# Performance work log

Hardware: AMD Instinct MI355X
Metric: run time of the kernel (lower is better)

The kernel has to match this reference:

```python
import jax, jax.numpy as jnp
import numpy as np

KSZ = 5   # local window size per spatial dim
NH = 4    # num_channels -> attention heads
EPS = 1e-6

def rmsnorm(x, w):
    return x * jax.lax.rsqrt(jnp.mean(x * x, axis=-1, keepdims=True) + EPS) * w

def local_windows(x, ksz):
    # x: [B, D, H, W, C] -> [B, D, H, W, ksz**3, C] zero-padded SAME windows
    B, D, H, Wd, C = x.shape
    xt = jnp.transpose(x, (0, 4, 1, 2, 3))  # NCDHW
    p = jax.lax.conv_general_dilated_patches(xt, (ksz, ksz, ksz), (1, 1, 1), 'SAME')
    p = p.reshape(B, C, ksz ** 3, D, H, Wd)  # channel-major patch layout
    return jnp.transpose(p, (0, 3, 4, 5, 2, 1))

def forward(x, norm1_w, attn_norm_w, norm2_w, wq, wk, wv, wo, gate_w, up_w, down_w):
    B, D, H, Wd, C = x.shape
    hd = C // NH
    k3 = KSZ ** 3
    h = rmsnorm(x, norm1_w)
    q = (h @ wq).reshape(B, D, H, Wd, NH, hd)
    k = h @ wk
    v = h @ wv
    kwin = local_windows(k, KSZ).reshape(B, D, H, Wd, k3, NH, hd)
    vwin = local_windows(v, KSZ).reshape(B, D, H, Wd, k3, NH, hd)
    scores = jnp.einsum('bxyzhe,bxyzkhe->bxyzhk', q, kwin) / jnp.sqrt(jnp.float32(hd))
    ones = jnp.ones((1, D, H, Wd, 1), x.dtype)
    valid = local_windows(ones, KSZ)[..., 0] > 0.5  # [1,D,H,W,k3] padding mask
    scores = jnp.where(valid[:, :, :, :, None, :], scores, jnp.float32(-1e9))
    attn = jax.nn.softmax(scores, axis=-1)
    o = jnp.einsum('bxyzhk,bxyzkhe->bxyzhe', attn, vwin).reshape(B, D, H, Wd, C)
    x = x + rmsnorm(o @ wo, attn_norm_w)
    h2 = rmsnorm(x, norm2_w)
    x = x + (jax.nn.silu(h2 @ gate_w) * (h2 @ up_w)) @ down_w  # SwiGLU (dropout=eval)
    return x

def setup_inputs():
    key = jax.random.key(0)
    ks = jax.random.split(key, 8)
    width, hidden = 128, 512
    s = 0.02
    return {
        'x': jax.random.normal(ks[0], (1, 16, 16, 16, width), jnp.float32),
        'norm1_w': jnp.ones((width,), jnp.float32),
        'attn_norm_w': jnp.ones((width,), jnp.float32),
        'norm2_w': jnp.ones((width,), jnp.float32),
        'wq': jax.random.normal(ks[1], (width, width), jnp.float32) * s,
        'wk': jax.random.normal(ks[2], (width, width), jnp.float32) * s,
        'wv': jax.random.normal(ks[3], (width, width), jnp.float32) * s,
        'wo': jax.random.normal(ks[4], (width, width), jnp.float32) * s,
        'gate_w': jax.random.normal(ks[5], (width, hidden), jnp.float32) * s,
        'up_w': jax.random.normal(ks[6], (width, hidden), jnp.float32) * s,
        'down_w': jax.random.normal(ks[7], (hidden, width), jnp.float32) * s,
    }

def reference(x, norm1_w, attn_norm_w, norm2_w, wq, wk, wv, wo, gate_w, up_w, down_w):
    return forward(x, norm1_w, attn_norm_w, norm2_w, wq, wk, wv, wo, gate_w, up_w, down_w)
```

## Files before the change

### kernel.cpp

```cpp
#include <hip/hip_runtime.h>
#include <hip/hip_bf16.h>

#define NVOX 4096
#define C    128
#define HID  512
#define EPSF 1e-6f

typedef __attribute__((ext_vector_type(8))) short bf16x8;
typedef __attribute__((ext_vector_type(4))) float f32x4;

__device__ __forceinline__ short f2bs(float f) {
    __hip_bfloat16 h = __float2bfloat16(f);
    short s; __builtin_memcpy(&s, &h, 2); return s;
}
__device__ __forceinline__ float bs2f(unsigned short u) {
    return __uint_as_float(((unsigned)u) << 16);
}

__device__ __forceinline__ bf16x8 lda(const short* hs, int lane, int ks) {
    int r = lane & 15, g = lane >> 4;
    int col = (ks * 32 + g * 8) ^ ((r & 7) << 3);
    return *(const bf16x8*)(hs + r * 128 + col);
}

__device__ __forceinline__ float wave_rsum(float s) {
    s += __shfl_xor(s, 32); s += __shfl_xor(s, 16); s += __shfl_xor(s, 8);
    s += __shfl_xor(s, 4);  s += __shfl_xor(s, 2);  s += __shfl_xor(s, 1);
    return s;
}

__global__ __launch_bounds__(512) void k_prep(
    const float* __restrict__ wq, const float* __restrict__ wk,
    const float* __restrict__ wv, const float* __restrict__ wo,
    const float* __restrict__ gw, const float* __restrict__ uw,
    const float* __restrict__ dw, short* __restrict__ wsw)
{
    int id = blockIdx.x * 512 + threadIdx.x;
    const float* src; int base, ct, ks, lane, N, KS;
    if (id < 8192) {
        int m = id >> 11, loc = id & 2047;
        src = (m == 0) ? wq : (m == 1) ? wk : (m == 2) ? wv : wo;
        base = m << 14; N = 128; KS = 4;
        ct = loc >> 8; ks = (loc >> 6) & 3; lane = loc & 63;
    } else if (id < 16384) {
        int loc = id - 8192;
        src = gw; base = 65536; N = 512; KS = 4;
        ct = loc >> 8; ks = (loc >> 6) & 3; lane = loc & 63;
    } else if (id < 24576) {
        int loc = id - 16384;
        src = uw; base = 131072; N = 512; KS = 4;
        ct = loc >> 8; ks = (loc >> 6) & 3; lane = loc & 63;
    } else {
        int loc = id - 24576;
        src = dw; base = 196608; N = 128; KS = 16;
        ct = loc >> 10; ks = (loc >> 6) & 15; lane = loc & 63;
    }
    int k0 = ks * 32 + (lane >> 4) * 8;
    int c  = ct * 16 + (lane & 15);
    bf16x8 v;
    #pragma unroll
    for (int j = 0; j < 8; j++) v[j] = f2bs(src[(size_t)(k0 + j) * N + c]);
    *(bf16x8*)(wsw + base + (((ct * KS + ks) * 64 + lane) << 3)) = v;
}

__global__ __launch_bounds__(256) void k_qkv(
    const float* __restrict__ x, const float* __restrict__ n1,
    const short* __restrict__ wsw,
    short* __restrict__ qbf, short* __restrict__ kbf, short* __restrict__ vbf)
{
    __shared__ short hs[2048];
    const int r0 = blockIdx.x * 16, t = threadIdx.x;
    const int w = t >> 6, lane = t & 63;

    #pragma unroll
    for (int i = 0; i < 4; i++) {
        int r = w * 4 + i;
        const float* xp = x + (size_t)(r0 + r) * 128;
        float v0 = xp[lane], v1 = xp[lane + 64];
        float s = wave_rsum(fmaf(v0, v0, v1 * v1));
        float sc = rsqrtf(s * (1.0f / 128.0f) + EPSF);
        int p3 = (r & 7) << 3;
        hs[r * 128 + (lane ^ p3)]        = f2bs(v0 * sc * n1[lane]);
        hs[r * 128 + ((lane + 64) ^ p3)] = f2bs(v1 * sc * n1[lane + 64]);
    }
    __syncthreads();

    bf16x8 af[4];
    #pragma unroll
    for (int ks = 0; ks < 4; ks++) af[ks] = lda(hs, lane, ks);

    const int rb = (lane >> 4) * 4, cl = lane & 15;
    #pragma unroll
    for (int m = 0; m < 3; m++) {
        const short* wb = wsw + (m << 14);
        f32x4 a0 = {0.f,0.f,0.f,0.f}, a1 = {0.f,0.f,0.f,0.f};
        #pragma unroll
        for (int ks = 0; ks < 4; ks++) {
            bf16x8 b0 = *(const bf16x8*)(wb + ((((w * 2) * 4 + ks) * 64 + lane) << 3));
            bf16x8 b1 = *(const bf16x8*)(wb + ((((w * 2 + 1) * 4 + ks) * 64 + lane) << 3));
            a0 = __builtin_amdgcn_mfma_f32_16x16x32_bf16(af[ks], b0, a0, 0, 0, 0);
            a1 = __builtin_amdgcn_mfma_f32_16x16x32_bf16(af[ks], b1, a1, 0, 0, 0);
        }
        short* outp = (m == 0) ? qbf : (m == 1) ? kbf : vbf;
        short* hp = outp + (size_t)w * NVOX * 32;
        #pragma unroll
        for (int i = 0; i < 4; i++) {
            hp[(size_t)(r0 + rb + i) * 32 + cl]      = f2bs(a0[i]);
            hp[(size_t)(r0 + rb + i) * 32 + 16 + cl] = f2bs(a1[i]);
        }
    }
}

__global__ __launch_bounds__(256) void k_attn(
    const short* __restrict__ qbf, const short* __restrict__ kbf,
    const short* __restrict__ vbf, short* __restrict__ obf)
{
    __shared__ __align__(16) char smem[64128];
    short* K_lds = (short*)smem;
    short* PA    = (short*)smem;
    short* S_lds = (short*)(smem + 30720);
    short* VB    = (short*)(smem + 30720);
    short* Q_lds = (short*)(smem + 61440);
    float* inv   = (float*)(smem + 64000);

    const int b = blockIdx.x, head = blockIdx.y, t = threadIdx.x;
    const int ow = (b & 3) * 4, oh = ((b >> 2) & 3) * 4, od = (b >> 4) * 2;
    const int w = t >> 6, lane = t & 63;
    const int g = lane >> 4, r = lane & 15;
    const short* kh = kbf + (size_t)head * NVOX * 32;
    const short* vh = vbf + (size_t)head * NVOX * 32;
    const short* qh = qbf + (size_t)head * NVOX * 32;

    uint4 v0[4] = {}, v1[4] = {};
    {
        int row = t;
        int lw = row & 7, lh = (row >> 3) & 7, ld = row >> 6;
        int gd = od - 2 + ld, gh = oh - 2 + lh, gw_ = ow - 2 + lw;
        int sv = (((unsigned)gd < 16u) && ((unsigned)gh < 16u) && ((unsigned)gw_ < 16u));
        size_t off = (size_t)((((gd << 4) | gh) << 4) | gw_) * 32;
        uint4 kc[4];
        #pragma unroll
        for (int c2 = 0; c2 < 4; c2++) {
            kc[c2] = sv ? *(const uint4*)(kh + off + c2 * 8) : (uint4){0,0,0,0};
            v0[c2] = sv ? *(const uint4*)(vh + off + c2 * 8) : (uint4){0,0,0,0};
        }
        #pragma unroll
        for (int c2 = 0; c2 < 4; c2++) *(uint4*)&K_lds[row * 40 + c2 * 8] = kc[c2];

        if (t >= 128) {
            int row1 = t + 128;
            int lw1 = row1 & 7, lh1 = (row1 >> 3) & 7, ld1 = row1 >> 6;
            int gd1 = od - 2 + ld1, gh1 = oh - 2 + lh1, gw1 = ow - 2 + lw1;
            int sv1 = (((unsigned)gd1 < 16u) && ((unsigned)gh1 < 16u) && ((unsigned)gw1 < 16u));
            size_t off1 = (size_t)((((gd1 << 4) | gh1) << 4) | gw1) * 32;
            uint4 kd[4];
            #pragma unroll
            for (int c2 = 0; c2 < 4; c2++) {
                kd[c2] = sv1 ? *(const uint4*)(kh + off1 + c2 * 8) : (uint4){0,0,0,0};
                v1[c2] = sv1 ? *(const uint4*)(vh + off1 + c2 * 8) : (uint4){0,0,0,0};
            }
            #pragma unroll
            for (int c2 = 0; c2 < 4; c2++) *(uint4*)&K_lds[row1 * 40 + c2 * 8] = kd[c2];
        } else {
            int q = t >> 2, c2q = t & 3;
            int gq = ((od + (q >> 4)) << 8) | ((oh + ((q >> 2) & 3)) << 4) | (ow + (q & 3));
            *(uint4*)&Q_lds[q * 40 + c2q * 8] = *(const uint4*)(qh + (size_t)gq * 32 + c2q * 8);
        }
    }
    __syncthreads();

    {
        bf16x8 bq0 = *(const bf16x8*)(Q_lds + r * 40 + g * 8);
        bf16x8 bq1 = *(const bf16x8*)(Q_lds + (16 + r) * 40 + g * 8);
        #pragma unroll
        for (int jj = 0; jj < 6; jj++) {
            int mt = w + jj * 4;
            bf16x8 ak = *(const bf16x8*)(K_lds + (mt * 16 + r) * 40 + g * 8);
            f32x4 a0 = {0.f,0.f,0.f,0.f}, a1 = {0.f,0.f,0.f,0.f};
            a0 = __builtin_amdgcn_mfma_f32_16x16x32_bf16(ak, bq0, a0, 0, 0, 0);
            a1 = __builtin_amdgcn_mfma_f32_16x16x32_bf16(ak, bq1, a1, 0, 0, 0);
            #pragma unroll
            for (int i = 0; i < 4; i++) {
                int key = mt * 16 + g * 4 + i;
                S_lds[key * 40 + r]      = f2bs(a0[i]);
                S_lds[key * 40 + 16 + r] = f2bs(a1[i]);
            }
        }
    }
    __syncthreads();

    {
        const int q = t >> 3, kl = t & 7;
        const int qw_ = q & 3, qh_ = (q >> 2) & 3, qd_ = q >> 4;
        const float isq = 0.17677669529663687f;
        float mx = -1e30f;
        #pragma unroll
        for (int j = 0; j < 48; j++) {
            int k = kl + (j << 3);
            int lw = k & 7, lh = (k >> 3) & 7, ld = k >> 6;
            int ok = ((unsigned)(ld - qd_) <= 4u) & ((unsigned)(lh - qh_) <= 4u)
                   & ((unsigned)(lw - qw_) <= 4u)
                   & ((unsigned)(od - 2 + ld) < 16u) & ((unsigned)(oh - 2 + lh) < 16u)
                   & ((unsigned)(ow - 2 + lw) < 16u);
            float s = bs2f((unsigned short)S_lds[k * 40 + q]) * isq;
            mx = ok ? fmaxf(mx, s) : mx;
        }
        mx = fmaxf(mx, __shfl_xor(mx, 1));
        mx = fmaxf(mx, __shfl_xor(mx, 2));
        mx = fmaxf(mx, __shfl_xor(mx, 4));
        float ssum = 0.f;
        const int pabase = (q >> 4) * 12 * 512 + (q & 15) * 8 + kl;
        #pragma unroll
        for (int j = 0; j < 48; j++) {
            int k = kl + (j << 3);
            int lw = k & 7, lh = (k >> 3) & 7, ld = k >> 6;
            int ok = ((unsigned)(ld - qd_) <= 4u) & ((unsigned)(lh - qh_) <= 4u)
                   & ((unsigned)(lw - qw_) <= 4u)
                   & ((unsigned)(od - 2 + ld) < 16u) & ((unsigned)(oh - 2 + lh) < 16u)
                   & ((unsigned)(ow - 2 + lw) < 16u);
            float s = bs2f((unsigned short)S_lds[k * 40 + q]) * isq;
            float p = ok ? __expf(s - mx) : 0.f;
            ssum += p;
            PA[pabase + (j >> 2) * 512 + (j & 3) * 128] = f2bs(p);
        }
        ssum += __shfl_xor(ssum, 1);
        ssum += __shfl_xor(ssum, 2);
        ssum += __shfl_xor(ssum, 4);
        if (kl == 0) inv[q] = 1.0f / ssum;
    }
    __syncthreads();

    {
        int row = t;
        int ks = row >> 5, g3 = (row >> 3) & 3, j3 = row & 7;
        const unsigned short* u = (const unsigned short*)v0;
        #pragma unroll
        for (int c = 0; c < 32; c++)
            VB[((c >> 4) * 12 + ks) * 512 + g3 * 128 + (c & 15) * 8 + j3] = (short)u[c];
        if (t >= 128) {
            int row1 = t + 128;
            int ks1 = row1 >> 5, g31 = (row1 >> 3) & 3, j31 = row1 & 7;
            const unsigned short* u1 = (const unsigned short*)v1;
            #pragma unroll
            for (int c = 0; c < 32; c++)
                VB[((c >> 4) * 12 + ks1) * 512 + g31 * 128 + (c & 15) * 8 + j31] = (short)u1[c];
        }
    }
    __syncthreads();

    {
        const int mt2 = w >> 1, ct = w & 1;
        f32x4 acc = {0.f,0.f,0.f,0.f};
        #pragma unroll
        for (int ks = 0; ks < 12; ks++) {
            bf16x8 pa = *(const bf16x8*)(PA + (((mt2 * 12 + ks) * 64 + lane) << 3));
            bf16x8 vb = *(const bf16x8*)(VB + (((ct * 12 + ks) * 64 + lane) << 3));
            acc = __builtin_amdgcn_mfma_f32_16x16x32_bf16(pa, vb, acc, 0, 0, 0);
        }
        #pragma unroll
        for (int i = 0; i < 4; i++) {
            int q = mt2 * 16 + g * 4 + i;
            int c = ct * 16 + r;
            int gvox = ((od + (q >> 4)) << 8) | ((oh + ((q >> 2) & 3)) << 4) | (ow + (q & 3));
            obf[(size_t)gvox * 128 + head * 32 + c] = f2bs(acc[i] * inv[q]);
        }
    }
}

__global__ __launch_bounds__(256) void k_post(
    const short* __restrict__ obf, const short* __restrict__ wsw,
    const float* __restrict__ anw, const float* __restrict__ x,
    const float* __restrict__ n2w, float* __restrict__ out)
{
    __shared__ float ybuf[16][132];
    __shared__ float xres[16][128];
    __shared__ short hs[2048];
    __shared__ short gu[16 * 512];

    const int r0 = blockIdx.x * 16, t = threadIdx.x;
    const int w = t >> 6, lane = t & 63;
    const int ar = lane & 15, ag_ = lane >> 4;

    {
        const short* wb = wsw + (3 << 14);
        f32x4 a0 = {0.f,0.f,0.f,0.f}, a1 = {0.f,0.f,0.f,0.f};
        #pragma unroll
        for (int ks = 0; ks < 4; ks++) {
            bf16x8 a = *(const bf16x8*)(obf + (size_t)(r0 + ar) * 128 + ks * 32 + ag_ * 8);
            bf16x8 b0 = *(const bf16x8*)(wb + ((((w * 2) * 4 + ks) * 64 + lane) << 3));
            bf16x8 b1 = *(const bf16x8*)(wb + ((((w * 2 + 1) * 4 + ks) * 64 + lane) << 3));
            a0 = __builtin_amdgcn_mfma_f32_16x16x32_bf16(a, b0, a0, 0, 0, 0);
            a1 = __builtin_amdgcn_mfma_f32_16x16x32_bf16(a, b1, a1, 0, 0, 0);
        }
        #pragma unroll
        for (int i = 0; i < 4; i++) {
            ybuf[ag_ * 4 + i][w * 32 + ar]      = a0[i];
            ybuf[ag_ * 4 + i][w * 32 + 16 + ar] = a1[i];
        }
    }
    __syncthreads();

    #pragma unroll
    for (int i = 0; i < 4; i++) {
        int r = w * 4 + i;
        float y0 = ybuf[r][lane], y1 = ybuf[r][lane + 64];
        float s = wave_rsum(fmaf(y0, y0, y1 * y1));
        float sc = rsqrtf(s * (1.0f / 128.0f) + EPSF);
        const float* xp = x + (size_t)(r0 + r) * 128;
        float xr0 = xp[lane]      + y0 * sc * anw[lane];
        float xr1 = xp[lane + 64] + y1 * sc * anw[lane + 64];
        xres[r][lane] = xr0; xres[r][lane + 64] = xr1;
        float s2 = wave_rsum(fmaf(xr0, xr0, xr1 * xr1));
        float sc2 = rsqrtf(s2 * (1.0f / 128.0f) + EPSF);
        int p3 = (r & 7) << 3;
        hs[r * 128 + (lane ^ p3)]        = f2bs(xr0 * sc2 * n2w[lane]);
        hs[r * 128 + ((lane + 64) ^ p3)] = f2bs(xr1 * sc2 * n2w[lane + 64]);
    }
    __syncthreads();

    {
        const short* gwb = wsw + 65536;
        const short* uwb = wsw + 131072;
        bf16x8 af[4];
        #pragma unroll
        for (int ks = 0; ks < 4; ks++) af[ks] = lda(hs, lane, ks);
        f32x4 ag[8], au[8];
        #pragma unroll
        for (int i = 0; i < 8; i++) { ag[i] = (f32x4){0.f,0.f,0.f,0.f}; au[i] = (f32x4){0.f,0.f,0.f,0.f}; }
        #pragma unroll
        for (int ks = 0; ks < 4; ks++) {
            #pragma unroll
            for (int i = 0; i < 8; i++) {
                int ct = w * 8 + i;
                bf16x8 bg = *(const bf16x8*)(gwb + (((ct * 4 + ks) * 64 + lane) << 3));
                bf16x8 bu = *(const bf16x8*)(uwb + (((ct * 4 + ks) * 64 + lane) << 3));
                ag[i] = __builtin_amdgcn_mfma_f32_16x16x32_bf16(af[ks], bg, ag[i], 0, 0, 0);
                au[i] = __builtin_amdgcn_mfma_f32_16x16x32_bf16(af[ks], bu, au[i], 0, 0, 0);
            }
        }
        #pragma unroll
        for (int i = 0; i < 8; i++) {
            int col = (w * 8 + i) * 16 + ar;
            #pragma unroll
            for (int j = 0; j < 4; j++) {
                int row = ag_ * 4 + j;
                float g = ag[i][j], uu = au[i][j];
                float sg = g / (1.0f + __expf(-g));
                gu[row * 512 + (col ^ ((row & 7) << 3))] = f2bs(sg * uu);
            }
        }
    }
    __syncthreads();

    {
        const short* db = wsw + 196608;
        f32x4 a0 = {0.f,0.f,0.f,0.f}, a1 = {0.f,0.f,0.f,0.f};
        #pragma unroll
        for (int ks = 0; ks < 16; ks++) {
            int col = (ks * 32 + ag_ * 8) ^ ((ar & 7) << 3);
            bf16x8 a = *(const bf16x8*)(gu + ar * 512 + col);
            bf16x8 b0 = *(const bf16x8*)(db + ((((w * 2) * 16 + ks) * 64 + lane) << 3));
            bf16x8 b1 = *(const bf16x8*)(db + ((((w * 2 + 1) * 16 + ks) * 64 + lane) << 3));
            a0 = __builtin_amdgcn_mfma_f32_16x16x32_bf16(a, b0, a0, 0, 0, 0);
            a1 = __builtin_amdgcn_mfma_f32_16x16x32_bf16(a, b1, a1, 0, 0, 0);
        }
        #pragma unroll
        for (int i = 0; i < 4; i++) {
            int row = ag_ * 4 + i;
            size_t i0 = (size_t)(r0 + row) * 128 + w * 32 + ar;
            out[i0]      = xres[row][w * 32 + ar]      + a0[i];
            out[i0 + 16] = xres[row][w * 32 + 16 + ar] + a1[i];
        }
    }
}

extern "C" void kernel_launch(void* const* d_in, const int* in_sizes, int n_in,
                              void* d_out, int out_size, void* d_ws, size_t ws_size,
                              hipStream_t stream)
{
    const float* x   = (const float*)d_in[0];
    const float* n1  = (const float*)d_in[1];
    const float* anw = (const float*)d_in[2];
    const float* n2  = (const float*)d_in[3];
    const float* wq  = (const float*)d_in[4];
    const float* wk  = (const float*)d_in[5];
    const float* wv  = (const float*)d_in[6];
    const float* wo  = (const float*)d_in[7];
    const float* gw  = (const float*)d_in[8];
    const float* uw  = (const float*)d_in[9];
    const float* dw  = (const float*)d_in[10];
    float* out = (float*)d_out;

    float* ws = (float*)d_ws;
    short* qbf = (short*)ws;
    short* kbf = (short*)(ws + 262144);
    short* vbf = (short*)(ws + 524288);
    short* obf = (short*)(ws + 786432);
    short* wsw = (short*)(ws + 1048576);

    k_prep<<<64,  512, 0, stream>>>(wq, wk, wv, wo, gw, uw, dw, wsw);
    k_qkv <<<256, 256, 0, stream>>>(x, n1, wsw, qbf, kbf, vbf);
    dim3 ga(128, 4);
    k_attn<<<ga,  256, 0, stream>>>(qbf, kbf, vbf, obf);
    k_post<<<256, 256, 0, stream>>>(obf, wsw, anw, x, n2, out);
}
```

Before: 37.50 us.

## Overlap weight conversion with QKV, transpose score layout, head-major attention output

Shrinks the weight-prep kernel to only the Q/K/V weights and moves conversion of wo, gate, up and down weights into the QKV kernel, spread across its blocks, so that work overlaps the QKV projection and the prep kernel finishes sooner. The attention score buffer is transposed to query-major, so each thread writes packed 64-bit stores and reads its scores with vector loads. The validity mask is computed once and kept in a bitmask rather than recomputed in the second softmax pass. The attention output is stored head-major, and the post kernel's A-operand loads change to match. The risk is extra register pressure and tail work in the QKV kernel.

```diff
diff --git a/kernel.cpp b/kernel.cpp
--- a/kernel.cpp
+++ b/kernel.cpp
@@ -31,46 +31,50 @@
 
 __global__ __launch_bounds__(512) void k_prep(
     const float* __restrict__ wq, const float* __restrict__ wk,
-    const float* __restrict__ wv, const float* __restrict__ wo,
-    const float* __restrict__ gw, const float* __restrict__ uw,
-    const float* __restrict__ dw, short* __restrict__ wsw)
+    const float* __restrict__ wv, short* __restrict__ wsw)
 {
     int id = blockIdx.x * 512 + threadIdx.x;
-    const float* src; int base, ct, ks, lane, N, KS;
-    if (id < 8192) {
-        int m = id >> 11, loc = id & 2047;
-        src = (m == 0) ? wq : (m == 1) ? wk : (m == 2) ? wv : wo;
-        base = m << 14; N = 128; KS = 4;
-        ct = loc >> 8; ks = (loc >> 6) & 3; lane = loc & 63;
-    } else if (id < 16384) {
-        int loc = id - 8192;
-        src = gw; base = 65536; N = 512; KS = 4;
-        ct = loc >> 8; ks = (loc >> 6) & 3; lane = loc & 63;
-    } else if (id < 24576) {
-        int loc = id - 16384;
-        src = uw; base = 131072; N = 512; KS = 4;
-        ct = loc >> 8; ks = (loc >> 6) & 3; lane = loc & 63;
-    } else {
-        int loc = id - 24576;
-        src = dw; base = 196608; N = 128; KS = 16;
-        ct = loc >> 10; ks = (loc >> 6) & 15; lane = loc & 63;
-    }
+    int m = id >> 11, loc = id & 2047;
+    const float* src = (m == 0) ? wq : (m == 1) ? wk : wv;
+    int base = m << 14;
+    int ct = loc >> 8, ks = (loc >> 6) & 3, lane = loc & 63;
     int k0 = ks * 32 + (lane >> 4) * 8;
     int c  = ct * 16 + (lane & 15);
     bf16x8 v;
     #pragma unroll
-    for (int j = 0; j < 8; j++) v[j] = f2bs(src[(size_t)(k0 + j) * N + c]);
-    *(bf16x8*)(wsw + base + (((ct * KS + ks) * 64 + lane) << 3)) = v;
+    for (int j = 0; j < 8; j++) v[j] = f2bs(src[(size_t)(k0 + j) * 128 + c]);
+    *(bf16x8*)(wsw + base + (((ct * 4 + ks) * 64 + lane) << 3)) = v;
 }
 
 __global__ __launch_bounds__(256) void k_qkv(
     const float* __restrict__ x, const float* __restrict__ n1,
-    const short* __restrict__ wsw,
+    const float* __restrict__ wo, const float* __restrict__ gw,
+    const float* __restrict__ uw, const float* __restrict__ dw,
+    short* __restrict__ wsw,
     short* __restrict__ qbf, short* __restrict__ kbf, short* __restrict__ vbf)
 {
     __shared__ short hs[2048];
     const int r0 = blockIdx.x * 16, t = threadIdx.x;
     const int w = t >> 6, lane = t & 63;
+
+    if (t < 104) {
+        int gid = 6144 + blockIdx.x * 104 + t;
+        const float* src; int base, ct, ks2, ln2, N, KS;
+        if (gid < 8192)       { int loc = gid & 2047;  src = wo; base = 3 << 14; N = 128; KS = 4;
+                                ct = loc >> 8; ks2 = (loc >> 6) & 3; ln2 = loc & 63; }
+        else if (gid < 16384) { int loc = gid - 8192;  src = gw; base = 65536;  N = 512; KS = 4;
+                                ct = loc >> 8; ks2 = (loc >> 6) & 3; ln2 = loc & 63; }
+        else if (gid < 24576) { int loc = gid - 16384; src = uw; base = 131072; N = 512; KS = 4;
+                                ct = loc >> 8; ks2 = (loc >> 6) & 3; ln2 = loc & 63; }
+        else                  { int loc = gid - 24576; src = dw; base = 196608; N = 128; KS = 16;
+                                ct = loc >> 10; ks2 = (loc >> 6) & 15; ln2 = loc & 63; }
+        int k0 = ks2 * 32 + (ln2 >> 4) * 8;
+        int c  = ct * 16 + (ln2 & 15);
+        bf16x8 v;
+        #pragma unroll
+        for (int j = 0; j < 8; j++) v[j] = f2bs(src[(size_t)(k0 + j) * N + c]);
+        *(bf16x8*)(wsw + base + (((ct * KS + ks2) * 64 + ln2) << 3)) = v;
+    }
 
     #pragma unroll
     for (int i = 0; i < 4; i++) {
@@ -118,7 +122,7 @@
     __shared__ __align__(16) char smem[64128];
     short* K_lds = (short*)smem;
     short* PA    = (short*)smem;
-    short* S_lds = (short*)(smem + 30720);
+    short* S2    = (short*)(smem + 30720);
     short* VB    = (short*)(smem + 30720);
     short* Q_lds = (short*)(smem + 61440);
     float* inv   = (float*)(smem + 64000);
@@ -130,6 +134,7 @@
     const short* kh = kbf + (size_t)head * NVOX * 32;
     const short* vh = vbf + (size_t)head * NVOX * 32;
     const short* qh = qbf + (size_t)head * NVOX * 32;
+    short* oh_ = obf + (size_t)head * NVOX * 32;
 
     uint4 v0[4] = {}, v1[4] = {};
     {
@@ -179,12 +184,16 @@
             f32x4 a0 = {0.f,0.f,0.f,0.f}, a1 = {0.f,0.f,0.f,0.f};
             a0 = __builtin_amdgcn_mfma_f32_16x16x32_bf16(ak, bq0, a0, 0, 0, 0);
             a1 = __builtin_amdgcn_mfma_f32_16x16x32_bf16(ak, bq1, a1, 0, 0, 0);
-            #pragma unroll
-            for (int i = 0; i < 4; i++) {
-                int key = mt * 16 + g * 4 + i;
-                S_lds[key * 40 + r]      = f2bs(a0[i]);
-                S_lds[key * 40 + 16 + r] = f2bs(a1[i]);
-            }
+            int key0 = mt * 16 + g * 4;
+            short s4[4];
+            #pragma unroll
+            for (int i = 0; i < 4; i++) s4[i] = f2bs(a0[i]);
+            unsigned long long pk0; __builtin_memcpy(&pk0, s4, 8);
+            *(unsigned long long*)&S2[r * 392 + key0] = pk0;
+            #pragma unroll
+            for (int i = 0; i < 4; i++) s4[i] = f2bs(a1[i]);
+            unsigned long long pk1; __builtin_memcpy(&pk1, s4, 8);
+            *(unsigned long long*)&S2[(16 + r) * 392 + key0] = pk1;
         }
     }
     __syncthreads();
@@ -193,35 +202,43 @@
         const int q = t >> 3, kl = t & 7;
         const int qw_ = q & 3, qh_ = (q >> 2) & 3, qd_ = q >> 4;
         const float isq = 0.17677669529663687f;
+        uint4 sraw[6];
+        #pragma unroll
+        for (int jj = 0; jj < 6; jj++)
+            sraw[jj] = *(const uint4*)&S2[q * 392 + kl * 48 + jj * 8];
+        unsigned long long okb = 0;
         float mx = -1e30f;
         #pragma unroll
-        for (int j = 0; j < 48; j++) {
-            int k = kl + (j << 3);
-            int lw = k & 7, lh = (k >> 3) & 7, ld = k >> 6;
-            int ok = ((unsigned)(ld - qd_) <= 4u) & ((unsigned)(lh - qh_) <= 4u)
-                   & ((unsigned)(lw - qw_) <= 4u)
-                   & ((unsigned)(od - 2 + ld) < 16u) & ((unsigned)(oh - 2 + lh) < 16u)
-                   & ((unsigned)(ow - 2 + lw) < 16u);
-            float s = bs2f((unsigned short)S_lds[k * 40 + q]) * isq;
-            mx = ok ? fmaxf(mx, s) : mx;
+        for (int jj = 0; jj < 6; jj++) {
+            const unsigned short* u = (const unsigned short*)&sraw[jj];
+            #pragma unroll
+            for (int e = 0; e < 8; e++) {
+                int k = kl * 48 + jj * 8 + e;
+                int lw = k & 7, lh = (k >> 3) & 7, ld = k >> 6;
+                int ok = ((unsigned)(ld - qd_) <= 4u) & ((unsigned)(lh - qh_) <= 4u)
+                       & ((unsigned)(lw - qw_) <= 4u)
+                       & ((unsigned)(od - 2 + ld) < 16u) & ((unsigned)(oh - 2 + lh) < 16u)
+                       & ((unsigned)(ow - 2 + lw) < 16u);
+                float s = bs2f(u[e]) * isq;
+                mx = ok ? fmaxf(mx, s) : mx;
+                okb |= ((unsigned long long)ok) << (jj * 8 + e);
+            }
         }
         mx = fmaxf(mx, __shfl_xor(mx, 1));
         mx = fmaxf(mx, __shfl_xor(mx, 2));
         mx = fmaxf(mx, __shfl_xor(mx, 4));
         float ssum = 0.f;
-        const int pabase = (q >> 4) * 12 * 512 + (q & 15) * 8 + kl;
-        #pragma unroll
-        for (int j = 0; j < 48; j++) {
-            int k = kl + (j << 3);
-            int lw = k & 7, lh = (k >> 3) & 7, ld = k >> 6;
-            int ok = ((unsigned)(ld - qd_) <= 4u) & ((unsigned)(lh - qh_) <= 4u)
-                   & ((unsigned)(lw - qw_) <= 4u)
-                   & ((unsigned)(od - 2 + ld) < 16u) & ((unsigned)(oh - 2 + lh) < 16u)
-                   & ((unsigned)(ow - 2 + lw) < 16u);
-            float s = bs2f((unsigned short)S_lds[k * 40 + q]) * isq;
-            float p = ok ? __expf(s - mx) : 0.f;
-            ssum += p;
-            PA[pabase + (j >> 2) * 512 + (j & 3) * 128] = f2bs(p);
+        #pragma unroll
+        for (int jj = 0; jj < 6; jj++) {
+            const unsigned short* u = (const unsigned short*)&sraw[jj];
+            #pragma unroll
+            for (int e = 0; e < 8; e++) {
+                int k = kl * 48 + jj * 8 + e;
+                float s = bs2f(u[e]) * isq;
+                float p = ((okb >> (jj * 8 + e)) & 1) ? __expf(s - mx) : 0.f;
+                ssum += p;
+                PA[((q >> 4) * 12 + (k >> 5)) * 512 + ((k >> 3) & 3) * 128 + (q & 15) * 8 + (k & 7)] = f2bs(p);
+            }
         }
         ssum += __shfl_xor(ssum, 1);
         ssum += __shfl_xor(ssum, 2);
@@ -262,7 +279,7 @@
             int q = mt2 * 16 + g * 4 + i;
             int c = ct * 16 + r;
             int gvox = ((od + (q >> 4)) << 8) | ((oh + ((q >> 2) & 3)) << 4) | (ow + (q & 3));
-            obf[(size_t)gvox * 128 + head * 32 + c] = f2bs(acc[i] * inv[q]);
+            oh_[(size_t)gvox * 32 + c] = f2bs(acc[i] * inv[q]);
         }
     }
 }
@@ -286,7 +303,7 @@
         f32x4 a0 = {0.f,0.f,0.f,0.f}, a1 = {0.f,0.f,0.f,0.f};
         #pragma unroll
         for (int ks = 0; ks < 4; ks++) {
-            bf16x8 a = *(const bf16x8*)(obf + (size_t)(r0 + ar) * 128 + ks * 32 + ag_ * 8);
+            bf16x8 a = *(const bf16x8*)(obf + (size_t)ks * NVOX * 32 + (size_t)(r0 + ar) * 32 + ag_ * 8);
             bf16x8 b0 = *(const bf16x8*)(wb + ((((w * 2) * 4 + ks) * 64 + lane) << 3));
             bf16x8 b1 = *(const bf16x8*)(wb + ((((w * 2 + 1) * 4 + ks) * 64 + lane) << 3));
             a0 = __builtin_amdgcn_mfma_f32_16x16x32_bf16(a, b0, a0, 0, 0, 0);
@@ -398,8 +415,8 @@
     short* obf = (short*)(ws + 786432);
     short* wsw = (short*)(ws + 1048576);
 
-    k_prep<<<64,  512, 0, stream>>>(wq, wk, wv, wo, gw, uw, dw, wsw);
-    k_qkv <<<256, 256, 0, stream>>>(x, n1, wsw, qbf, kbf, vbf);
+    k_prep<<<12,  512, 0, stream>>>(wq, wk, wv, wsw);
+    k_qkv <<<256, 256, 0, stream>>>(x, n1, wo, gw, uw, dw, wsw, qbf, kbf, vbf);
     dim3 ga(128, 4);
     k_attn<<<ga,  256, 0, stream>>>(qbf, kbf, vbf, obf);
     k_post<<<256, 256, 0, stream>>>(obf, wsw, anw, x, n2, out);
```

Result: faster. 36.74 us (-2.0%).
